# Kernel tuning notes

Hardware: AMD Instinct MI355X
Metric: run time of the kernel (lower is better)

## Reference

```python
import jax, jax.numpy as jnp
import numpy as np

B, L, T, V = 32, 200, 500, 80
DM, DE = 256, 512
D4 = 4 * DM              # 1024 (decoder LSTM width)
R = 2                    # reduction rate
STEPS = T // R           # 250 decoder steps
KSIZE, PADC, NFILT, DA = 31, 15, 32, 128
ZONEOUT, KEEP = 0.1, 0.5
MAXSTEP = 500            # hard-coded attention buffer length


def setup_inputs() -> dict:
    key = jax.random.key(0)
    ks = jax.random.split(key, 24)
    def lin(k, fan_in, shape):
        s = 1.0 / np.sqrt(fan_in)
        return jax.random.uniform(k, shape, minval=-s, maxval=s, dtype=jnp.float32)
    return {
        'meltarget': jax.random.normal(ks[0], (B, T, V), jnp.float32),
        'e_outputs': jax.random.normal(ks[1], (B, L, DE), jnp.float32),
        'conv_w':    lin(ks[2], KSIZE, (NFILT, 1, KSIZE)),
        'W_convproj': lin(ks[3], NFILT, (NFILT, DA)),
        'W_encproj': lin(ks[4], DE, (DE, DA)), 'b_encproj': lin(ks[5], DE, (DA,)),
        'W_decproj': lin(ks[6], D4, (D4, DA)),
        'W_self':    lin(ks[7], DA, (DA,)),
        'W_pre1': lin(ks[8], V, (V, DM)),   'b_pre1': lin(ks[9], V, (DM,)),
        'W_pre2': lin(ks[10], DM, (DM, DM)), 'b_pre2': lin(ks[11], DM, (DM,)),
        'W_l1_ys': lin(ks[12], DM, (DM, 4 * D4)),
        'W_l1_ss': lin(ks[13], D4, (D4, 4 * D4)),
        'W_l1_gs': lin(ks[14], 2 * DM, (2 * DM, 4 * D4)), 'b_l1_gs': lin(ks[15], 2 * DM, (4 * D4,)),
        'W_l2_is': lin(ks[16], D4, (D4, 4 * D4)),
        'W_l2_ss': lin(ks[17], D4, (D4, 4 * D4)), 'b_l2_ss': lin(ks[18], D4, (4 * D4,)),
        'W_frame': lin(ks[19], D4 + 2 * DM, (D4 + 2 * DM, V * R)), 'b_frame': lin(ks[20], D4 + 2 * DM, (V * R,)),
        'W_token': lin(ks[21], D4 + 2 * DM, (D4 + 2 * DM, R)),     'b_token': lin(ks[22], D4 + 2 * DM, (R,)),
    }


def _gate(x):
    # tanh(x*0.5)*0.5 + 0.5 == sigmoid(x), kept in the original's form
    return jnp.tanh(x * 0.5) * 0.5 + 0.5


def reference(meltarget, e_outputs, conv_w, W_convproj, W_encproj, b_encproj,
              W_decproj, W_self, W_pre1, b_pre1, W_pre2, b_pre2,
              W_l1_ys, W_l1_ss, W_l1_gs, b_l1_gs, W_l2_is, W_l2_ss, b_l2_ss,
              W_frame, b_frame, W_token, b_token):
    base_key = jax.random.key(1234)
    encproj = e_outputs @ W_encproj + b_encproj              # [B,L,DA], step-invariant
    mel_last = jnp.transpose(meltarget[:, R - 1::R, :], (1, 0, 2))  # [STEPS,B,V]

    def step_fn(carry, xs):
        prev_pred, cum_alpha, s1, c1, s2, c2 = carry
        step, mel_t = xs
        kd1, kd2, kz1, kz2 = jax.random.split(jax.random.fold_in(base_key, step), 4)
        # location-sensitive attention
        ac = jax.lax.conv_general_dilated(
            cum_alpha[:, None, :], conv_w, (1,), [(PADC, PADC)],
            dimension_numbers=('NCH', 'OIH', 'NCH'))         # [B,32,L]
        attconv = jnp.einsum('bfl,fa->bla', ac, W_convproj)  # [B,L,DA]
        decproj = (s2 @ W_decproj)[:, None, :]               # [B,1,DA]
        e = jnp.tanh(decproj + encproj + attconv)
        score = e @ W_self                                   # [B,L]
        alpha = jax.nn.softmax(score, axis=1)
        cum_alpha = cum_alpha + alpha
        g = jnp.einsum('bl,bld->bd', alpha, e_outputs)       # [B,DE]
        # prenet with dropout p=0.5
        pre1 = jax.nn.relu(prev_pred @ W_pre1 + b_pre1)
        pre1 = pre1 * jax.random.bernoulli(kd1, KEEP, pre1.shape) / KEEP
        pre2 = jax.nn.relu(pre1 @ W_pre2 + b_pre2)
        pre2 = pre2 * jax.random.bernoulli(kd2, KEEP, pre2.shape) / KEEP
        # LSTM cell 1 with zoneout
        rec = pre2 @ W_l1_ys + s1 @ W_l1_ss + g @ W_l1_gs + b_l1_gs
        i1, f1, cg1, o1 = jnp.split(rec, 4, axis=1)
        m1 = jnp.floor(jax.random.uniform(kz1, (B, D4)) + ZONEOUT)  # Bernoulli(zoneout) keep-old mask
        c1n = m1 * c1 + (1.0 - m1) * (_gate(f1) * c1 + _gate(i1) * jnp.tanh(cg1))
        s1n = m1 * s1 + (1.0 - m1) * (_gate(o1) * jnp.tanh(c1n))
        # LSTM cell 2 with zoneout
        rec2 = s1n @ W_l2_is + s2 @ W_l2_ss + b_l2_ss
        i2, f2, cg2, o2 = jnp.split(rec2, 4, axis=1)
        m2 = jnp.floor(jax.random.uniform(kz2, (B, D4)) + ZONEOUT)
        c2n = m2 * c2 + (1.0 - m2) * (_gate(f2) * c2 + _gate(i2) * jnp.tanh(cg2))
        s2n = m2 * s2 + (1.0 - m2) * (_gate(o2) * jnp.tanh(c2n))
        proj_in = jnp.concatenate([s2n, g], axis=1)          # [B, D4+2*DM]
        frame = proj_in @ W_frame + b_frame                  # [B, R*V]
        token = proj_in @ W_token + b_token                  # [B, R]
        return (mel_t, cum_alpha, s1n, c1n, s2n, c2n), (frame, token, alpha)

    z = jnp.zeros((B, D4), jnp.float32)
    carry0 = (jnp.zeros((B, V), jnp.float32), jnp.zeros((B, L), jnp.float32), z, z, z, z)
    _, (frames, tokens, alphas) = jax.lax.scan(step_fn, carry0, (jnp.arange(STEPS), mel_last))
    frame_sent = jnp.transpose(frames, (1, 0, 2)).reshape(B, STEPS * R, V)
    token_sent = jnp.transpose(tokens, (1, 0, 2)).reshape(B, STEPS * R)
    attn = jnp.zeros((B, MAXSTEP, L), jnp.float32).at[:, :STEPS].set(
        jax.lax.stop_gradient(jnp.transpose(alphas, (1, 0, 2))))
    return frame_sent, token_sent, attn
```

## Files before the change

kernel.cpp:

```cpp
#include <hip/hip_runtime.h>
#include <cstdint>
#include <cstddef>


static constexpr int NSTEP = 250;

static constexpr size_t OFF_ENCPROJ = 0;
static constexpr size_t OFF_CWT     = 819200;
static constexpr size_t OFF_KEYS    = 823296;
static constexpr size_t OFF_PRE2    = 825344;
static constexpr size_t OFF_G       = 2873344;
static constexpr size_t OFF_S2      = 6969344;
static constexpr size_t OFF_S1      = 15194112;
static constexpr size_t OFF_C1      = 15259648;
static constexpr size_t OFF_C2      = 15292416;
static constexpr size_t OFF_CUM     = 15325184;
static constexpr size_t OFF_DPART   = 15333376;
static constexpr size_t OFF_SC      = 15366144;
static constexpr size_t OFF_P1      = 15390720;
static constexpr size_t OFF_P2      = 17225728;

static constexpr size_t OUT_TOK  = 1280000;
static constexpr size_t OUT_ATTN = 1296000;

__device__ __forceinline__ uint2 threefry(unsigned k0, unsigned k1, unsigned c0, unsigned c1) {
  unsigned ks2 = k0 ^ k1 ^ 0x1BD11BDAu;
  unsigned x0 = c0 + k0, x1 = c1 + k1;
#define TFR(rot) { x0 += x1; x1 = (x1 << (rot)) | (x1 >> (32 - (rot))); x1 ^= x0; }
  TFR(13) TFR(15) TFR(26) TFR(6)   x0 += k1;  x1 += ks2 + 1u;
  TFR(17) TFR(29) TFR(16) TFR(24)  x0 += ks2; x1 += k0 + 2u;
  TFR(13) TFR(15) TFR(26) TFR(6)   x0 += k0;  x1 += k1 + 3u;
  TFR(17) TFR(29) TFR(16) TFR(24)  x0 += k1;  x1 += ks2 + 4u;
  TFR(13) TFR(15) TFR(26) TFR(6)   x0 += ks2; x1 += k0 + 5u;
#undef TFR
  return make_uint2(x0, x1);
}

__device__ __forceinline__ float u32_to_uniform(unsigned b) {
  return __uint_as_float((b >> 9) | 0x3f800000u) - 1.0f;
}

__device__ __forceinline__ float rng_uniform(unsigned k0, unsigned k1, unsigned i) {
  uint2 h = threefry(k0, k1, 0u, i);
  return u32_to_uniform(h.x ^ h.y);
}

__device__ __forceinline__ float gatef(float x) { return tanhf(x * 0.5f) * 0.5f + 0.5f; }

#define FMA4(A, S, W) { (A).x = fmaf((S), (W).x, (A).x); (A).y = fmaf((S), (W).y, (A).y); \
                        (A).z = fmaf((S), (W).z, (A).z); (A).w = fmaf((S), (W).w, (A).w); }

__global__ __launch_bounds__(256) void k_init(float* __restrict__ ws, float* __restrict__ out,
                                              const float* __restrict__ conv_w,
                                              const float* __restrict__ Wcp) {
  const size_t NZERO1 = 172032;
  const size_t NZERO2 = 32768;
  const size_t NATTN  = 1600000;
  const size_t NKEYS  = 250;
  const size_t NCWT   = 4096;
  const size_t TOTAL  = NZERO1 + NZERO2 + NATTN + NKEYS + NCWT;
  unsigned* keys = (unsigned*)(ws + OFF_KEYS);
  for (size_t i = (size_t)blockIdx.x * 256 + threadIdx.x; i < TOTAL; i += (size_t)gridDim.x * 256) {
    if (i < NZERO1) {
      ws[OFF_S1 + i] = 0.f;
    } else if (i < NZERO1 + NZERO2) {
      ws[OFF_S2 + (i - NZERO1)] = 0.f;
    } else if (i < NZERO1 + NZERO2 + NATTN) {
      size_t r = i - NZERO1 - NZERO2;
      size_t b = r / 50000, rem = r % 50000;
      out[OUT_ATTN + b * 100000 + 50000 + rem] = 0.f;
    } else if (i < NZERO1 + NZERO2 + NATTN + NKEYS) {
      int s = (int)(i - NZERO1 - NZERO2 - NATTN);
      uint2 F = threefry(0u, 1234u, 0u, (unsigned)s);
      uint2 kd1 = threefry(F.x, F.y, 0u, 0u);
      uint2 kd2 = threefry(F.x, F.y, 0u, 1u);
      uint2 kz1 = threefry(F.x, F.y, 0u, 2u);
      uint2 kz2 = threefry(F.x, F.y, 0u, 3u);
      keys[s * 8 + 0] = kd1.x; keys[s * 8 + 1] = kd1.y;
      keys[s * 8 + 2] = kd2.x; keys[s * 8 + 3] = kd2.y;
      keys[s * 8 + 4] = kz1.x; keys[s * 8 + 5] = kz1.y;
      keys[s * 8 + 6] = kz2.x; keys[s * 8 + 7] = kz2.y;
    } else {
      size_t r = i - NZERO1 - NZERO2 - NATTN - NKEYS;
      int a = (int)(r >> 5), kk = (int)(r & 31);
      float v = 0.f;
      if (kk < 31) {
        for (int f = 0; f < 32; ++f) v = fmaf(conv_w[f * 31 + kk], Wcp[f * 128 + a], v);
      }
      ws[OFF_CWT + r] = v;
    }
  }
}

__global__ __launch_bounds__(256) void k_encproj(const float* __restrict__ e_out,
                                                 const float* __restrict__ Wenc,
                                                 const float* __restrict__ benc,
                                                 float* __restrict__ encproj) {
  __shared__ __align__(16) float xs[32 * 516];
  int t = threadIdx.x;
  int r0 = blockIdx.x * 32;
  for (int i = 0; i < 64; ++i) {
    int idx = t + 256 * i; int rb = idx >> 9, kk = idx & 511;
    xs[rb * 516 + kk] = e_out[(size_t)(r0 + rb) * 512 + kk];
  }
  __syncthreads();
  int a = t & 127, rh = t >> 7;
  float acc[16];
#pragma unroll
  for (int r = 0; r < 16; ++r) acc[r] = 0.f;
  const float4* xv = (const float4*)xs;
  for (int k4 = 0; k4 < 128; ++k4) {
    const float* wp = Wenc + (size_t)(k4 * 4) * 128 + a;
    float w0 = wp[0], w1 = wp[128], w2 = wp[256], w3 = wp[384];
#pragma unroll
    for (int r = 0; r < 16; ++r) {
      float4 x4 = xv[(rh * 16 + r) * 129 + k4];
      acc[r] = fmaf(x4.x, w0, acc[r]); acc[r] = fmaf(x4.y, w1, acc[r]);
      acc[r] = fmaf(x4.z, w2, acc[r]); acc[r] = fmaf(x4.w, w3, acc[r]);
    }
  }
  float bb = benc[a];
  for (int r = 0; r < 16; ++r)
    encproj[(size_t)(r0 + rh * 16 + r) * 128 + a] = acc[r] + bb;
}

__global__ __launch_bounds__(256) void k_prenet(const float* __restrict__ mel,
                                                const float* __restrict__ W1, const float* __restrict__ b1,
                                                const float* __restrict__ W2, const float* __restrict__ b2,
                                                const unsigned* __restrict__ keys,
                                                float* __restrict__ pre2_all) {
  int s = blockIdx.x, t = threadIdx.x;
  __shared__ __align__(16) float prev[32 * 80];
  __shared__ __align__(16) float p1[32 * 256];
  for (int i = 0; i < 10; ++i) {
    int idx = t + 256 * i;
    int bb = idx / 80, vv = idx % 80;
    prev[idx] = (s == 0) ? 0.f : mel[(size_t)bb * 40000 + (size_t)(2 * s - 1) * 80 + vv];
  }
  __syncthreads();
  unsigned kd10 = keys[s * 8 + 0], kd11 = keys[s * 8 + 1];
  unsigned kd20 = keys[s * 8 + 2], kd21 = keys[s * 8 + 3];
  float acc[32];
  float bias = b1[t];
#pragma unroll
  for (int b = 0; b < 32; ++b) acc[b] = bias;
  for (int k4 = 0; k4 < 20; ++k4) {
    const float* wp = W1 + (size_t)(k4 * 4) * 256 + t;
    float w0 = wp[0], w1 = wp[256], w2 = wp[512], w3 = wp[768];
#pragma unroll
    for (int b = 0; b < 32; ++b) {
      float4 x4 = *(const float4*)(prev + b * 80 + k4 * 4);
      acc[b] = fmaf(x4.x, w0, acc[b]); acc[b] = fmaf(x4.y, w1, acc[b]);
      acc[b] = fmaf(x4.z, w2, acc[b]); acc[b] = fmaf(x4.w, w3, acc[b]);
    }
  }
#pragma unroll
  for (int b = 0; b < 32; ++b) {
    float r = fmaxf(acc[b], 0.f);
    float u = rng_uniform(kd10, kd11, (unsigned)(b * 256 + t));
    p1[b * 256 + t] = (u < 0.5f) ? r * 2.f : 0.f;
  }
  __syncthreads();
  float bias2 = b2[t];
#pragma unroll
  for (int b = 0; b < 32; ++b) acc[b] = bias2;
  for (int k4 = 0; k4 < 64; ++k4) {
    const float* wp = W2 + (size_t)(k4 * 4) * 256 + t;
    float w0 = wp[0], w1 = wp[256], w2 = wp[512], w3 = wp[768];
#pragma unroll
    for (int b = 0; b < 32; ++b) {
      float4 x4 = *(const float4*)(p1 + b * 256 + k4 * 4);
      acc[b] = fmaf(x4.x, w0, acc[b]); acc[b] = fmaf(x4.y, w1, acc[b]);
      acc[b] = fmaf(x4.z, w2, acc[b]); acc[b] = fmaf(x4.w, w3, acc[b]);
    }
  }
  for (int b = 0; b < 32; ++b) {
    float r = fmaxf(acc[b], 0.f);
    float u = rng_uniform(kd20, kd21, (unsigned)(b * 256 + t));
    pre2_all[(size_t)(s * 32 + b) * 256 + t] = (u < 0.5f) ? r * 2.f : 0.f;
  }
}

__global__ __launch_bounds__(256) void k_escore(const float* __restrict__ dpart,
                                                const float* __restrict__ encproj,
                                                const float* __restrict__ cwt,
                                                const float* __restrict__ cum,
                                                const float* __restrict__ Wself,
                                                float* __restrict__ sglob) {
  int b = blockIdx.x & 31, p = blockIdx.x >> 5;
  int t = threadIdx.x;
  __shared__ float dp[128];
  __shared__ float ca[232];
  __shared__ float scpart[4];
  if (t < 128) {
    float acc = 0.f;
#pragma unroll
    for (int q = 0; q < 8; ++q) acc += dpart[(b * 8 + q) * 128 + t];
    dp[t] = acc;
  }
  if (t < 232) ca[t] = (t >= 15 && t < 215) ? cum[b * 200 + (t - 15)] : 0.f;
  __syncthreads();
  int a = t & 127, lh = t >> 7;
  float cwr[31];
#pragma unroll
  for (int k = 0; k < 31; ++k) cwr[k] = cwt[a * 32 + k];
  float wself = Wself[a];
  float dpr = dp[a];
  for (int ii = 0; ii < 13; ++ii) {
    int lo = ii * 2 + lh;
    int l = p * 25 + lo;
    float v = 0.f;
    if (lo < 25) {
      float conv = 0.f;
#pragma unroll
      for (int k = 0; k < 31; ++k) conv = fmaf(ca[l + k], cwr[k], conv);
      float e = tanhf(dpr + encproj[(size_t)(b * 200 + l) * 128 + a] + conv);
      v = e * wself;
    }
#pragma unroll
    for (int off = 32; off > 0; off >>= 1) v += __shfl_xor(v, off, 64);
    if ((t & 63) == 0) scpart[t >> 6] = v;
    __syncthreads();
    if (t == 0) sglob[b * 200 + p * 25 + ii * 2] = scpart[0] + scpart[1];
    if (t == 128 && ii < 12) sglob[b * 200 + p * 25 + ii * 2 + 1] = scpart[2] + scpart[3];
    __syncthreads();
  }
}

__global__ __launch_bounds__(256) void k_attng(const float* __restrict__ sglob,
                                               const float* __restrict__ e_out,
                                               float* __restrict__ cum,
                                               float* __restrict__ g_out,
                                               float* __restrict__ attn_out) {
  int b = blockIdx.x & 31, p = blockIdx.x >> 5;
  int t = threadIdx.x;
  __shared__ float sc[200];
  __shared__ float red[8];
  __shared__ float bcv[2];
  __shared__ float gpart[4][64];
  if (t < 200) sc[t] = sglob[b * 200 + t];
  __syncthreads();
  float v = (t < 200) ? sc[t] : -3.4e38f;
#pragma unroll
  for (int off = 32; off > 0; off >>= 1) v = fmaxf(v, __shfl_xor(v, off, 64));
  if ((t & 63) == 0) red[t >> 6] = v;
  __syncthreads();
  if (t == 0) bcv[0] = fmaxf(fmaxf(red[0], red[1]), fmaxf(red[2], red[3]));
  __syncthreads();
  float mx = bcv[0];
  float ex = (t < 200) ? expf(sc[t] - mx) : 0.f;
  float sv = ex;
#pragma unroll
  for (int off = 32; off > 0; off >>= 1) sv += __shfl_xor(sv, off, 64);
  if ((t & 63) == 0) red[4 + (t >> 6)] = sv;
  __syncthreads();
  if (t == 0) bcv[1] = (red[4] + red[5]) + (red[6] + red[7]);
  __syncthreads();
  float denom = bcv[1];
  if (t < 200) {
    float al = ex / denom;
    sc[t] = al;
    if (p == 0) {
      cum[b * 200 + t] += al;
      attn_out[(size_t)b * 100000 + t] = al;
    }
  }
  __syncthreads();
  int d = p * 64 + (t & 63), lq = t >> 6;
  const float* eb = e_out + (size_t)b * 102400 + d;
  float acc = 0.f;
  for (int l = lq * 50; l < lq * 50 + 50; ++l) acc = fmaf(sc[l], eb[(size_t)l * 512], acc);
  gpart[lq][t & 63] = acc;
  __syncthreads();
  if (t < 64)
    g_out[b * 512 + p * 64 + t] = (gpart[0][t] + gpart[1][t]) + (gpart[2][t] + gpart[3][t]);
}

__device__ __forceinline__ void gemm_body(
    const float* __restrict__ W0, int k0,
    float* __restrict__ part, int c, int jt,
    const float* __restrict__ xs ) {
  int t = threadIdx.x;
  int jq = t & 31, bq = t >> 5;
  int j = jt * 32 + jq;
  float4 acc[4];
  acc[0] = acc[1] = acc[2] = acc[3] = make_float4(0, 0, 0, 0);
  const float4* xv = (const float4*)xs;
  const float* Wb = W0 + (size_t)k0 * 4096 + j;
#pragma unroll 4
  for (int k4 = 0; k4 < 32; ++k4) {
    float4 xq[4];
    xq[0] = xv[(bq * 4 + 0) * 33 + k4];
    xq[1] = xv[(bq * 4 + 1) * 33 + k4];
    xq[2] = xv[(bq * 4 + 2) * 33 + k4];
    xq[3] = xv[(bq * 4 + 3) * 33 + k4];
    const float* wr = Wb + (size_t)(k4 * 4) * 4096;
#pragma unroll
    for (int ks = 0; ks < 4; ++ks) {
      float wi = wr[0], wf = wr[1024], wc = wr[2048], wo = wr[3072];
      wr += 4096;
#pragma unroll
      for (int r = 0; r < 4; ++r) {
        float xval = ((const float*)&xq[r])[ks];
        acc[r].x = fmaf(xval, wi, acc[r].x);
        acc[r].y = fmaf(xval, wf, acc[r].y);
        acc[r].z = fmaf(xval, wc, acc[r].z);
        acc[r].w = fmaf(xval, wo, acc[r].w);
      }
    }
  }
  float* pb = part + (size_t)c * 131072 + (size_t)(bq * 4) * 4096 + j;
#pragma unroll
  for (int r = 0; r < 4; ++r) {
    float* pr = pb + r * 4096;
    pr[0] = acc[r].x; pr[1024] = acc[r].y; pr[2048] = acc[r].z; pr[3072] = acc[r].w;
  }
}

__global__ __launch_bounds__(256) void k_b1g(
    const float* __restrict__ pre2_s, const float* __restrict__ s1old,
    const float* __restrict__ g_s,
    const float* __restrict__ Wys, const float* __restrict__ Wss, const float* __restrict__ Wgs,
    float* __restrict__ part) {
  int t = threadIdx.x;
  int jt = blockIdx.x & 31, c = blockIdx.x >> 5;
  __shared__ __align__(16) float xs[32 * 132];
  {
    int r = t >> 3, kq = t & 7;
    const float* src;
    if (c < 2)       src = pre2_s + r * 256 + c * 128;
    else if (c < 10) src = s1old + r * 1024 + (c - 2) * 128;
    else             src = g_s + r * 512 + (c - 10) * 128;
    const float4* s4 = (const float4*)(src + kq * 16);
    float4* d4 = (float4*)(xs + r * 132 + kq * 16);
    d4[0] = s4[0]; d4[1] = s4[1]; d4[2] = s4[2]; d4[3] = s4[3];
  }
  const float* W0; int k0;
  if (c < 2)       { W0 = Wys; k0 = c * 128; }
  else if (c < 10) { W0 = Wss; k0 = (c - 2) * 128; }
  else             { W0 = Wgs; k0 = (c - 10) * 128; }
  __syncthreads();
  gemm_body(W0, k0, part, c, jt, xs);
}

__global__ __launch_bounds__(256) void k_b2g(
    const float* __restrict__ s1new, const float* __restrict__ s2prev,
    const float* __restrict__ Wis, const float* __restrict__ Wss2,
    float* __restrict__ part) {
  int t = threadIdx.x;
  int jt = blockIdx.x & 31, c = blockIdx.x >> 5;
  __shared__ __align__(16) float xs[32 * 132];
  {
    int r = t >> 3, kq = t & 7;
    const float* src = (c < 8) ? (s1new + r * 1024 + c * 128)
                               : (s2prev + r * 1024 + (c - 8) * 128);
    const float4* s4 = (const float4*)(src + kq * 16);
    float4* d4 = (float4*)(xs + r * 132 + kq * 16);
    d4[0] = s4[0]; d4[1] = s4[1]; d4[2] = s4[2]; d4[3] = s4[3];
  }
  const float* W0; int k0;
  if (c < 8) { W0 = Wis;  k0 = c * 128; }
  else       { W0 = Wss2; k0 = (c - 8) * 128; }
  __syncthreads();
  gemm_body(W0, k0, part, c, jt, xs);
}

__global__ __launch_bounds__(256) void k_cell1(
    const float* __restrict__ part, const float* __restrict__ bias,
    const float* __restrict__ sold, float* __restrict__ snew, float* __restrict__ cst,
    const unsigned* __restrict__ keyp) {
  int e = blockIdx.x * 256 + threadIdx.x;
  int b = e >> 10, j = e & 1023;
  float gi = bias[j], gf = bias[1024 + j], gc = bias[2048 + j], go = bias[3072 + j];
  const float* pc = part + (size_t)b * 4096 + j;
#pragma unroll
  for (int cc = 0; cc < 14; ++cc) {
    const float* p2 = pc + (size_t)cc * 131072;
    gi += p2[0]; gf += p2[1024]; gc += p2[2048]; go += p2[3072];
  }
  float u = rng_uniform(keyp[0], keyp[1], (unsigned)e);
  float m = floorf(u + 0.1f);
  float co = cst[e], so = sold[e];
  float cn = fmaf(gatef(gf), co, gatef(gi) * tanhf(gc));
  float cnew = (m > 0.5f) ? co : cn;
  float sn = (m > 0.5f) ? so : (gatef(go) * tanhf(cnew));
  cst[e] = cnew;
  snew[e] = sn;
}

__global__ __launch_bounds__(256) void k_cell2dp(
    const float* __restrict__ part, const float* __restrict__ bias,
    const float* __restrict__ sold, float* __restrict__ snew, float* __restrict__ cst,
    const unsigned* __restrict__ keyp,
    const float* __restrict__ Wdec, float* __restrict__ dpart) {
  int b = blockIdx.x & 31, p = blockIdx.x >> 5;
  int t = threadIdx.x;
  __shared__ float s2l[128];
  __shared__ float dtmp[256];
  if (t < 128) {
    int j = p * 128 + t;
    int e = b * 1024 + j;
    float gi = bias[j], gf = bias[1024 + j], gc = bias[2048 + j], go = bias[3072 + j];
    const float* pc = part + (size_t)b * 4096 + j;
#pragma unroll
    for (int cc = 0; cc < 16; ++cc) {
      const float* p2 = pc + (size_t)cc * 131072;
      gi += p2[0]; gf += p2[1024]; gc += p2[2048]; go += p2[3072];
    }
    float u = rng_uniform(keyp[0], keyp[1], (unsigned)e);
    float m = floorf(u + 0.1f);
    float co = cst[e], so = sold[e];
    float cn = fmaf(gatef(gf), co, gatef(gi) * tanhf(gc));
    float cnew = (m > 0.5f) ? co : cn;
    float sn = (m > 0.5f) ? so : (gatef(go) * tanhf(cnew));
    cst[e] = cnew;
    snew[e] = sn;
    s2l[t] = sn;
  }
  __syncthreads();
  int a = t & 127, h = t >> 7;
  const float* wp = Wdec + (size_t)(p * 128 + h * 64) * 128 + a;
  float acc = 0.f;
#pragma unroll 8
  for (int r = 0; r < 64; ++r) acc = fmaf(s2l[h * 64 + r], wp[(size_t)r * 128], acc);
  dtmp[t] = acc;
  __syncthreads();
  if (t < 128) dpart[(b * 8 + p) * 128 + t] = dtmp[t] + dtmp[t + 128];
}

__global__ __launch_bounds__(256) void k_frame(const float* __restrict__ s2_all,
                                               const float* __restrict__ g_all,
                                               const float* __restrict__ Wf,
                                               const float* __restrict__ bf,
                                               const float* __restrict__ Wt,
                                               const float* __restrict__ bt,
                                               float* __restrict__ out_frame,
                                               float* __restrict__ out_tok) {
  int s = blockIdx.x, t = threadIdx.x;
  __shared__ __align__(16) float xs[32 * 516];
  int b = t >> 3, ci = t & 7;
  int tb = t >> 1, tr = t & 1;
  float4 acc[5];
#pragma unroll
  for (int r = 0; r < 5; ++r) acc[r] = make_float4(0, 0, 0, 0);
  float tok = 0.f;
  for (int ch = 0; ch < 3; ++ch) {
    for (int i = 0; i < 64; ++i) {
      int idx = t + 256 * i;
      int rb = idx >> 9, kk = idx & 511;
      float vsrc = (ch < 2) ? s2_all[(size_t)(s + 1) * 32768 + rb * 1024 + ch * 512 + kk]
                            : g_all[(size_t)s * 16384 + rb * 512 + kk];
      xs[rb * 516 + kk] = vsrc;
    }
    __syncthreads();
    const float4* xv = (const float4*)xs;
    for (int k4 = 0; k4 < 128; ++k4) {
      float4 x4 = xv[b * 129 + k4];
      int kglob = ch * 512 + k4 * 4;
#pragma unroll
      for (int rep = 0; rep < 5; ++rep) {
        int c4 = ci * 4 + rep * 32;
        const float* wrow = Wf + (size_t)kglob * 160 + c4;
        float4 w0 = *(const float4*)(wrow);
        float4 w1 = *(const float4*)(wrow + 160);
        float4 w2 = *(const float4*)(wrow + 320);
        float4 w3 = *(const float4*)(wrow + 480);
        FMA4(acc[rep], x4.x, w0); FMA4(acc[rep], x4.y, w1);
        FMA4(acc[rep], x4.z, w2); FMA4(acc[rep], x4.w, w3);
      }
      if (t < 64) {
        float4 xt = xv[tb * 129 + k4];
        tok = fmaf(xt.x, Wt[(size_t)(kglob + 0) * 2 + tr], tok);
        tok = fmaf(xt.y, Wt[(size_t)(kglob + 1) * 2 + tr], tok);
        tok = fmaf(xt.z, Wt[(size_t)(kglob + 2) * 2 + tr], tok);
        tok = fmaf(xt.w, Wt[(size_t)(kglob + 3) * 2 + tr], tok);
      }
    }
    __syncthreads();
  }
#pragma unroll
  for (int rep = 0; rep < 5; ++rep) {
    float vals[4] = {acc[rep].x, acc[rep].y, acc[rep].z, acc[rep].w};
#pragma unroll
    for (int jj = 0; jj < 4; ++jj) {
      int cc = ci * 4 + rep * 32 + jj;
      float val = vals[jj] + bf[cc];
      int row = 2 * s + (cc >= 80 ? 1 : 0);
      int col = cc - (cc >= 80 ? 80 : 0);
      out_frame[(size_t)b * 40000 + (size_t)row * 80 + col] = val;
    }
  }
  if (t < 64) out_tok[(size_t)tb * 500 + 2 * s + tr] = tok + bt[tr];
}

extern "C" void kernel_launch(void* const* d_in, const int* in_sizes, int n_in,
                              void* d_out_v, int out_size, void* d_ws, size_t ws_size,
                              hipStream_t stream) {
  (void)in_sizes; (void)n_in; (void)out_size; (void)ws_size;
  const float* mel      = (const float*)d_in[0];
  const float* e_out    = (const float*)d_in[1];
  const float* conv_w   = (const float*)d_in[2];
  const float* Wcp      = (const float*)d_in[3];
  const float* Wenc     = (const float*)d_in[4];
  const float* benc     = (const float*)d_in[5];
  const float* Wdec     = (const float*)d_in[6];
  const float* Wself    = (const float*)d_in[7];
  const float* Wp1      = (const float*)d_in[8];
  const float* bp1      = (const float*)d_in[9];
  const float* Wp2      = (const float*)d_in[10];
  const float* bp2      = (const float*)d_in[11];
  const float* Wys      = (const float*)d_in[12];
  const float* Wss      = (const float*)d_in[13];
  const float* Wgs      = (const float*)d_in[14];
  const float* bgs      = (const float*)d_in[15];
  const float* Wis      = (const float*)d_in[16];
  const float* Wss2     = (const float*)d_in[17];
  const float* bss2     = (const float*)d_in[18];
  const float* Wf       = (const float*)d_in[19];
  const float* bf       = (const float*)d_in[20];
  const float* Wt       = (const float*)d_in[21];
  const float* bt       = (const float*)d_in[22];
  float* ws  = (float*)d_ws;
  float* out = (float*)d_out_v;
  const unsigned* keys = (const unsigned*)(ws + OFF_KEYS);

  hipLaunchKernelGGL(k_init, dim3(1024), dim3(256), 0, stream, ws, out, conv_w, Wcp);
  hipLaunchKernelGGL(k_encproj, dim3(200), dim3(256), 0, stream, e_out, Wenc, benc, ws + OFF_ENCPROJ);
  hipLaunchKernelGGL(k_prenet, dim3(250), dim3(256), 0, stream, mel, Wp1, bp1, Wp2, bp2, keys, ws + OFF_PRE2);

  for (int s = 0; s < NSTEP; ++s) {
    float* s1old = ws + OFF_S1 + (size_t)(s & 1) * 32768;
    float* s1new = ws + OFF_S1 + (size_t)((s + 1) & 1) * 32768;
    float* s2s   = ws + OFF_S2 + (size_t)s * 32768;
    float* s2n   = ws + OFF_S2 + (size_t)(s + 1) * 32768;
    float* gs    = ws + OFF_G  + (size_t)s * 16384;
    hipLaunchKernelGGL(k_escore, dim3(256), dim3(256), 0, stream,
                       ws + OFF_DPART, ws + OFF_ENCPROJ, ws + OFF_CWT, ws + OFF_CUM,
                       Wself, ws + OFF_SC);
    hipLaunchKernelGGL(k_attng, dim3(256), dim3(256), 0, stream,
                       ws + OFF_SC, e_out, ws + OFF_CUM, gs,
                       out + OUT_ATTN + (size_t)s * 200);
    hipLaunchKernelGGL(k_b1g, dim3(448), dim3(256), 0, stream,
                       ws + OFF_PRE2 + (size_t)s * 8192, s1old, gs, Wys, Wss, Wgs,
                       ws + OFF_P1);
    hipLaunchKernelGGL(k_cell1, dim3(128), dim3(256), 0, stream,
                       ws + OFF_P1, bgs, s1old, s1new, ws + OFF_C1, keys + s * 8 + 4);
    hipLaunchKernelGGL(k_b2g, dim3(512), dim3(256), 0, stream,
                       s1new, s2s, Wis, Wss2, ws + OFF_P2);
    hipLaunchKernelGGL(k_cell2dp, dim3(256), dim3(256), 0, stream,
                       ws + OFF_P2, bss2, s2s, s2n, ws + OFF_C2, keys + s * 8 + 6,
                       Wdec, ws + OFF_DPART);
  }
  hipLaunchKernelGGL(k_frame, dim3(250), dim3(256), 0, stream,
                     ws + OFF_S2, ws + OFF_G, Wf, bf, Wt, bt, out, out + OUT_TOK);
}
```

Measured before the change: 15.50 ms.

## Fuse LSTM2 cell update and decoder projection into next step's attention score kernel

Removes the per-step cell2/decoder-projection kernel. Each step's attention-score kernel now recomputes the previous step's second LSTM cell and the full 1024x128 decoder projection inside every block, which drops one launch per step and the dpart round trip through global memory. The c2 state is ping-ponged between two buffers, and a final standalone cell kernel finishes the last step. In exchange, each of the 8 blocks per batch row redundantly does the full cell and matvec, with a long serial per-thread dot product on half the threads. That could lengthen the critical path more than the saved launch overhead.

```diff
diff --git a/kernel.cpp b/kernel.cpp
--- a/kernel.cpp
+++ b/kernel.cpp
@@ -13,9 +13,9 @@
 static constexpr size_t OFF_S2      = 6969344;
 static constexpr size_t OFF_S1      = 15194112;
 static constexpr size_t OFF_C1      = 15259648;
-static constexpr size_t OFF_C2      = 15292416;
+static constexpr size_t OFF_C2     = 15292416;
 static constexpr size_t OFF_CUM     = 15325184;
-static constexpr size_t OFF_DPART   = 15333376;
+static constexpr size_t OFF_C2B     = 15333376;
 static constexpr size_t OFF_SC      = 15366144;
 static constexpr size_t OFF_P1      = 15390720;
 static constexpr size_t OFF_P2      = 17225728;
@@ -181,24 +181,67 @@
   }
 }
 
-__global__ __launch_bounds__(256) void k_escore(const float* __restrict__ dpart,
-                                                const float* __restrict__ encproj,
-                                                const float* __restrict__ cwt,
-                                                const float* __restrict__ cum,
-                                                const float* __restrict__ Wself,
-                                                float* __restrict__ sglob) {
+__global__ __launch_bounds__(256) void k_escore2(
+    int s,
+    const float* __restrict__ part,
+    const float* __restrict__ bias2,
+    const float* __restrict__ s2old,
+    float* __restrict__ s2new,
+    const float* __restrict__ c2old,
+    float* __restrict__ c2new,
+    const unsigned* __restrict__ keys,
+    const float* __restrict__ Wdec,
+    const float* __restrict__ encproj,
+    const float* __restrict__ cwt,
+    const float* __restrict__ cum,
+    const float* __restrict__ Wself,
+    float* __restrict__ sglob) {
   int b = blockIdx.x & 31, p = blockIdx.x >> 5;
   int t = threadIdx.x;
+  __shared__ float s2l[1024];
   __shared__ float dp[128];
   __shared__ float ca[232];
   __shared__ float scpart[4];
+  if (s > 0) {
+    const unsigned* keyp = keys + (size_t)(s - 1) * 8 + 6;
+    unsigned kk0 = keyp[0], kk1 = keyp[1];
+    for (int i = t; i < 1024; i += 256) {
+      int e = b * 1024 + i;
+      float gi = bias2[i], gf = bias2[1024 + i], gc = bias2[2048 + i], go = bias2[3072 + i];
+      const float* pc = part + (size_t)b * 4096 + i;
+#pragma unroll
+      for (int cc = 0; cc < 16; ++cc) {
+        const float* p2 = pc + (size_t)cc * 131072;
+        gi += p2[0]; gf += p2[1024]; gc += p2[2048]; go += p2[3072];
+      }
+      float u = rng_uniform(kk0, kk1, (unsigned)e);
+      float m = floorf(u + 0.1f);
+      float co = c2old[e], so = s2old[e];
+      float cn = fmaf(gatef(gf), co, gatef(gi) * tanhf(gc));
+      float cnew = (m > 0.5f) ? co : cn;
+      float sn = (m > 0.5f) ? so : (gatef(go) * tanhf(cnew));
+      c2new[e] = cnew;
+      s2new[e] = sn;
+      s2l[i] = sn;
+    }
+  } else {
+    for (int i = t; i < 1024; i += 256) s2l[i] = 0.f;
+  }
+  if (t < 232) ca[t] = (t >= 15 && t < 215) ? cum[b * 200 + (t - 15)] : 0.f;
+  __syncthreads();
   if (t < 128) {
     float acc = 0.f;
-#pragma unroll
-    for (int q = 0; q < 8; ++q) acc += dpart[(b * 8 + q) * 128 + t];
+    for (int q = 0; q < 8; ++q) {
+      const float* wp = Wdec + (size_t)(q * 128) * 128 + t;
+      float a0 = 0.f, a1 = 0.f;
+#pragma unroll 8
+      for (int r = 0; r < 64; ++r) a0 = fmaf(s2l[q * 128 + r], wp[(size_t)r * 128], a0);
+#pragma unroll 8
+      for (int r = 64; r < 128; ++r) a1 = fmaf(s2l[q * 128 + r], wp[(size_t)r * 128], a1);
+      acc += a0 + a1;
+    }
     dp[t] = acc;
   }
-  if (t < 232) ca[t] = (t >= 15 && t < 215) ? cum[b * 200 + (t - 15)] : 0.f;
   __syncthreads();
   int a = t & 127, lh = t >> 7;
   float cwr[31];
@@ -388,44 +431,28 @@
   snew[e] = sn;
 }
 
-__global__ __launch_bounds__(256) void k_cell2dp(
+__global__ __launch_bounds__(256) void k_cellfin(
     const float* __restrict__ part, const float* __restrict__ bias,
-    const float* __restrict__ sold, float* __restrict__ snew, float* __restrict__ cst,
-    const unsigned* __restrict__ keyp,
-    const float* __restrict__ Wdec, float* __restrict__ dpart) {
-  int b = blockIdx.x & 31, p = blockIdx.x >> 5;
-  int t = threadIdx.x;
-  __shared__ float s2l[128];
-  __shared__ float dtmp[256];
-  if (t < 128) {
-    int j = p * 128 + t;
-    int e = b * 1024 + j;
-    float gi = bias[j], gf = bias[1024 + j], gc = bias[2048 + j], go = bias[3072 + j];
-    const float* pc = part + (size_t)b * 4096 + j;
-#pragma unroll
-    for (int cc = 0; cc < 16; ++cc) {
-      const float* p2 = pc + (size_t)cc * 131072;
-      gi += p2[0]; gf += p2[1024]; gc += p2[2048]; go += p2[3072];
-    }
-    float u = rng_uniform(keyp[0], keyp[1], (unsigned)e);
-    float m = floorf(u + 0.1f);
-    float co = cst[e], so = sold[e];
-    float cn = fmaf(gatef(gf), co, gatef(gi) * tanhf(gc));
-    float cnew = (m > 0.5f) ? co : cn;
-    float sn = (m > 0.5f) ? so : (gatef(go) * tanhf(cnew));
-    cst[e] = cnew;
-    snew[e] = sn;
-    s2l[t] = sn;
-  }
-  __syncthreads();
-  int a = t & 127, h = t >> 7;
-  const float* wp = Wdec + (size_t)(p * 128 + h * 64) * 128 + a;
-  float acc = 0.f;
-#pragma unroll 8
-  for (int r = 0; r < 64; ++r) acc = fmaf(s2l[h * 64 + r], wp[(size_t)r * 128], acc);
-  dtmp[t] = acc;
-  __syncthreads();
-  if (t < 128) dpart[(b * 8 + p) * 128 + t] = dtmp[t] + dtmp[t + 128];
+    const float* __restrict__ sold, float* __restrict__ snew,
+    const float* __restrict__ c2old, float* __restrict__ c2new,
+    const unsigned* __restrict__ keyp) {
+  int e = blockIdx.x * 256 + threadIdx.x;
+  int b = e >> 10, j = e & 1023;
+  float gi = bias[j], gf = bias[1024 + j], gc = bias[2048 + j], go = bias[3072 + j];
+  const float* pc = part + (size_t)b * 4096 + j;
+#pragma unroll
+  for (int cc = 0; cc < 16; ++cc) {
+    const float* p2 = pc + (size_t)cc * 131072;
+    gi += p2[0]; gf += p2[1024]; gc += p2[2048]; go += p2[3072];
+  }
+  float u = rng_uniform(keyp[0], keyp[1], (unsigned)e);
+  float m = floorf(u + 0.1f);
+  float co = c2old[e], so = sold[e];
+  float cn = fmaf(gatef(gf), co, gatef(gi) * tanhf(gc));
+  float cnew = (m > 0.5f) ? co : cn;
+  float sn = (m > 0.5f) ? so : (gatef(go) * tanhf(cnew));
+  c2new[e] = cnew;
+  snew[e] = sn;
 }
 
 __global__ __launch_bounds__(256) void k_frame(const float* __restrict__ s2_all,
@@ -531,11 +558,14 @@
   for (int s = 0; s < NSTEP; ++s) {
     float* s1old = ws + OFF_S1 + (size_t)(s & 1) * 32768;
     float* s1new = ws + OFF_S1 + (size_t)((s + 1) & 1) * 32768;
-    float* s2s   = ws + OFF_S2 + (size_t)s * 32768;
-    float* s2n   = ws + OFF_S2 + (size_t)(s + 1) * 32768;
+    float* s2old = ws + OFF_S2 + (size_t)(s > 0 ? s - 1 : 0) * 32768;
+    float* s2cur = ws + OFF_S2 + (size_t)s * 32768;
     float* gs    = ws + OFF_G  + (size_t)s * 16384;
-    hipLaunchKernelGGL(k_escore, dim3(256), dim3(256), 0, stream,
-                       ws + OFF_DPART, ws + OFF_ENCPROJ, ws + OFF_CWT, ws + OFF_CUM,
+    float* c2old = ws + (((s - 1) & 1) ? OFF_C2B : OFF_C2);
+    float* c2new = ws + ((s & 1) ? OFF_C2B : OFF_C2);
+    hipLaunchKernelGGL(k_escore2, dim3(256), dim3(256), 0, stream,
+                       s, ws + OFF_P2, bss2, s2old, s2cur, c2old, c2new,
+                       keys, Wdec, ws + OFF_ENCPROJ, ws + OFF_CWT, ws + OFF_CUM,
                        Wself, ws + OFF_SC);
     hipLaunchKernelGGL(k_attng, dim3(256), dim3(256), 0, stream,
                        ws + OFF_SC, e_out, ws + OFF_CUM, gs,
@@ -546,11 +576,12 @@
     hipLaunchKernelGGL(k_cell1, dim3(128), dim3(256), 0, stream,
                        ws + OFF_P1, bgs, s1old, s1new, ws + OFF_C1, keys + s * 8 + 4);
     hipLaunchKernelGGL(k_b2g, dim3(512), dim3(256), 0, stream,
-                       s1new, s2s, Wis, Wss2, ws + OFF_P2);
-    hipLaunchKernelGGL(k_cell2dp, dim3(256), dim3(256), 0, stream,
-                       ws + OFF_P2, bss2, s2s, s2n, ws + OFF_C2, keys + s * 8 + 6,
-                       Wdec, ws + OFF_DPART);
-  }
+                       s1new, s2cur, Wis, Wss2, ws + OFF_P2);
+  }
+  hipLaunchKernelGGL(k_cellfin, dim3(128), dim3(256), 0, stream,
+                     ws + OFF_P2, bss2, ws + OFF_S2 + (size_t)249 * 32768,
+                     ws + OFF_S2 + (size_t)250 * 32768,
+                     ws + OFF_C2B, ws + OFF_C2, keys + 249 * 8 + 6);
   hipLaunchKernelGGL(k_frame, dim3(250), dim3(256), 0, stream,
                      ws + OFF_S2, ws + OFF_G, Wf, bf, Wt, bt, out, out + OUT_TOK);
 }
```

Measured after the change: 24.47 ms. 57.9% more time.
